# Kernel tuning notes

Hardware: AMD Instinct MI355X
Metric: run time of the kernel (lower is better)

Reference implementation:

```python
import jax, jax.numpy as jnp
import numpy as np

NB = 16   # num_blocks
DIN = 64  # per-block input dim
DOUT = 64 # per-block output dim
NT = 2    # n_templates (ns)


def setup_inputs() -> dict:
    key = jax.random.key(0)
    k1, k2, k3, k4, k5 = jax.random.split(key, 5)
    T, B = 2048, 8
    a = 0.1  # GroupLinearLayer init range
    x = jax.random.normal(k1, (T, B, NB * DIN), dtype=jnp.float32)
    module_emb = 0.1 * jax.random.normal(k2, (1, 1, NB * DIN), dtype=jnp.float32)
    read_w = jax.random.uniform(k3, (1, DIN, NT), dtype=jnp.float32, minval=-a, maxval=a)
    lim = 1.0 / np.sqrt(DIN)  # nn.Linear default init range
    w_stack = jax.random.uniform(k4, (NT, DOUT, DIN), dtype=jnp.float32, minval=-lim, maxval=lim)
    b_stack = jax.random.uniform(k5, (NT, DOUT), dtype=jnp.float32, minval=-lim, maxval=lim)
    return {"x": x, "module_emb": module_emb, "read_w": read_w,
            "w_stack": w_stack, "b_stack": b_stack}


def reference(x, module_emb, read_w, w_stack, b_stack):
    T, B, D = x.shape
    # add module embedding (broadcast over T, B)
    new_x = x + module_emb
    # flatten to per-block tokens: (N, DIN) with N = T*B*NB
    xf = new_x.reshape(T * B * NB, DIN)
    # routing logits via GroupLinearLayer with 1 block: (N, NT)
    logits = xf @ read_w[0]
    att = jax.nn.softmax(logits, axis=-1)
    # apply each template Linear: (N, NT, DOUT)
    x_next = jnp.einsum('nd,tod->nto', xf, w_stack) + b_stack[None, :, :]
    # soft combine templates; mean over singleton dim is identity
    out = jnp.einsum('nt,nto->no', att, x_next)
    return out.reshape(T, B, NB * DOUT)
```

## Files before the change

### kernel.cpp

```cpp
#include <hip/hip_runtime.h>


#define NBLK   768
#define WAVES  (NBLK * 4)
#define NTILES 16384

typedef short bf16x8 __attribute__((ext_vector_type(8)));
typedef float f32x4  __attribute__((ext_vector_type(4)));

union B8 { bf16x8 v; unsigned u[4]; };

__device__ __forceinline__ unsigned pk2bf(float lo, float hi) {
    unsigned a = __float_as_uint(lo) + 0x8000u;
    unsigned b = __float_as_uint(hi) + 0x8000u;
    return __builtin_amdgcn_perm(b, a, 0x07060302u);
}

__device__ __forceinline__ void pack8(B8& d, float4 p, float4 q) {
    d.u[0] = pk2bf(p.x, p.y); d.u[1] = pk2bf(p.z, p.w);
    d.u[2] = pk2bf(q.x, q.y); d.u[3] = pk2bf(q.z, q.w);
}

__global__ __launch_bounds__(256, 3) void sgll_kernel(
    const float* __restrict__ x,
    const float* __restrict__ emb,
    const float* __restrict__ rw,
    const float* __restrict__ ws,
    const float* __restrict__ bs,
    float* __restrict__ out)
{
    __shared__ bf16x8 sW1[8][64];
    __shared__ bf16x8 sWd[8][64];

    const int tid  = threadIdx.x;
    const int lane = tid & 63;
    const int wv   = tid >> 6;
    const int col  = lane & 15;
    const int q    = lane >> 4;

    #pragma unroll
    for (int c = wv; c < 8; c += 4) {
        const int kt = c >> 2, ot = c & 3;
        const float* p0 = ws + (ot * 16 + col) * 64 + kt * 32 + q * 8;
        const float* p1 = p0 + 4096;
        float4 a0 = *(const float4*)p0, a1 = *(const float4*)(p0 + 4);
        float4 c0 = *(const float4*)p1, c1 = *(const float4*)(p1 + 4);
        B8 f1, fd;
        pack8(f1, c0, c1);
        fd.u[0] = pk2bf(a0.x - c0.x, a0.y - c0.y);
        fd.u[1] = pk2bf(a0.z - c0.z, a0.w - c0.w);
        fd.u[2] = pk2bf(a1.x - c1.x, a1.y - c1.y);
        fd.u[3] = pk2bf(a1.z - c1.z, a1.w - c1.w);
        sW1[c][lane] = f1.v;
        sWd[c][lane] = fd.v;
    }

    B8 R0, R1;
    {
        const int c01 = col & 1;
        float v[8];
        #pragma unroll
        for (int j = 0; j < 8; ++j)
            v[j] = rw[(q * 8 + j) * 2 + c01];
        pack8(R0, make_float4(v[0], v[1], v[2], v[3]), make_float4(v[4], v[5], v[6], v[7]));
        #pragma unroll
        for (int j = 0; j < 8; ++j)
            v[j] = rw[(32 + q * 8 + j) * 2 + c01];
        pack8(R1, make_float4(v[0], v[1], v[2], v[3]), make_float4(v[4], v[5], v[6], v[7]));
    }

    B8 E0, E1;
    {
        const float* ep = emb + col * 64 + q * 8;
        pack8(E0, *(const float4*)ep, *(const float4*)(ep + 4));
        pack8(E1, *(const float4*)(ep + 32), *(const float4*)(ep + 36));
    }
    f32x4 bI1[4], bId[4];
    #pragma unroll
    for (int ot = 0; ot < 4; ++ot) {
        float4 b1 = *(const float4*)(bs + 64 + ot * 16 + q * 4);
        float4 b0 = *(const float4*)(bs + ot * 16 + q * 4);
        bI1[ot][0] = b1.x; bI1[ot][1] = b1.y; bI1[ot][2] = b1.z; bI1[ot][3] = b1.w;
        bId[ot][0] = b0.x - b1.x; bId[ot][1] = b0.y - b1.y;
        bId[ot][2] = b0.z - b1.z; bId[ot][3] = b0.w - b1.w;
    }

    __syncthreads();

    const int w = blockIdx.x * 4 + wv;

    auto loadt = [&](float4 (&B)[4], int T) {
        const float* p = x + ((long)T * 16 + col) * 64 + q * 8;
        B[0] = *(const float4*)p;        B[1] = *(const float4*)(p + 4);
        B[2] = *(const float4*)(p + 32); B[3] = *(const float4*)(p + 36);
    };

    float4 bA[4], bB[4], bC[4], bD[4];
    loadt(bA, w);
    loadt(bB, w + WAVES);
    loadt(bC, w + 2 * WAVES);
    loadt(bD, w + 3 * WAVES);
    __builtin_amdgcn_sched_barrier(0);

    f32x4 I1[4], Id[4], Il;
    #pragma unroll
    for (int ot = 0; ot < 4; ++ot) {
        f32x4 a1 = bI1[ot], ad = bId[ot];
        a1 = __builtin_amdgcn_mfma_f32_16x16x32_bf16(sW1[ot][lane],     E0.v, a1, 0, 0, 0);
        a1 = __builtin_amdgcn_mfma_f32_16x16x32_bf16(sW1[4 + ot][lane], E1.v, a1, 0, 0, 0);
        ad = __builtin_amdgcn_mfma_f32_16x16x32_bf16(sWd[ot][lane],     E0.v, ad, 0, 0, 0);
        ad = __builtin_amdgcn_mfma_f32_16x16x32_bf16(sWd[4 + ot][lane], E1.v, ad, 0, 0, 0);
        I1[ot] = a1;
        Id[ot] = ad;
    }
    {
        f32x4 z = {0.f, 0.f, 0.f, 0.f};
        z = __builtin_amdgcn_mfma_f32_16x16x32_bf16(R0.v, E0.v, z, 0, 0, 0);
        z = __builtin_amdgcn_mfma_f32_16x16x32_bf16(R1.v, E1.v, z, 0, 0, 0);
        Il = z;
    }

    auto step = [&](float4 (&B)[4], int TI, bool refill, int RT) {
        B8 X0, X1;
        pack8(X0, B[0], B[1]);
        pack8(X1, B[2], B[3]);
        if (refill) loadt(B, RT);

        f32x4 lac = Il;
        lac = __builtin_amdgcn_mfma_f32_16x16x32_bf16(R0.v, X0.v, lac, 0, 0, 0);
        lac = __builtin_amdgcn_mfma_f32_16x16x32_bf16(R1.v, X1.v, lac, 0, 0, 0);
        const float att = 1.0f / (1.0f + __expf(lac[1] - lac[0]));

        const long rowoff = ((long)TI * 16 + col) * 64;
        #pragma unroll
        for (int ot = 0; ot < 4; ++ot) {
            f32x4 y = I1[ot];
            y = __builtin_amdgcn_mfma_f32_16x16x32_bf16(sW1[ot][lane],     X0.v, y, 0, 0, 0);
            y = __builtin_amdgcn_mfma_f32_16x16x32_bf16(sW1[4 + ot][lane], X1.v, y, 0, 0, 0);
            f32x4 d = Id[ot];
            d = __builtin_amdgcn_mfma_f32_16x16x32_bf16(sWd[ot][lane],     X0.v, d, 0, 0, 0);
            d = __builtin_amdgcn_mfma_f32_16x16x32_bf16(sWd[4 + ot][lane], X1.v, d, 0, 0, 0);
            float4 o;
            o.x = fmaf(att, d[0], y[0]);
            o.y = fmaf(att, d[1], y[1]);
            o.z = fmaf(att, d[2], y[2]);
            o.w = fmaf(att, d[3], y[3]);
            *(float4*)(out + rowoff + ot * 16 + q * 4) = o;
        }
    };

    const bool six = (w < NTILES - 5 * WAVES);

    step(bA, w,             true, w + 4 * WAVES);
    step(bB, w +     WAVES, six,  w + 5 * WAVES);
    step(bC, w + 2 * WAVES, false, 0);
    step(bD, w + 3 * WAVES, false, 0);
    step(bA, w + 4 * WAVES, false, 0);
    if (six)
        step(bB, w + 5 * WAVES, false, 0);
}

extern "C" void kernel_launch(void* const* d_in, const int* in_sizes, int n_in,
                              void* d_out, int out_size, void* d_ws, size_t ws_size,
                              hipStream_t stream) {
    const float* x   = (const float*)d_in[0];
    const float* emb = (const float*)d_in[1];
    const float* rw  = (const float*)d_in[2];
    const float* wsk = (const float*)d_in[3];
    const float* bs  = (const float*)d_in[4];
    float* out = (float*)d_out;
    sgll_kernel<<<NBLK, 256, 0, stream>>>(x, emb, rw, wsk, bs, out);
}
```

Measured before the change: 137.5 us.

## Stage output tiles through swizzled LDS for coalesced stores, raise occupancy

Each wave now writes its 16x64 output tile into a per-wave LDS buffer with an XOR swizzle, then reads it back so each lane stores contiguous 16-byte chunks of whole rows, giving fully coalesced global writes. The prefetch depth drops from four to two tiles in flight per wave, the grid grows to 1280 blocks and launch bounds allow 5 blocks per CU, trading per-wave latency hiding for more resident waves. The extra LDS round trip adds work and 16 KB of shared memory per block, and the shallower prefetch may expose more load latency.

```diff
diff --git a/kernel.cpp b/kernel.cpp
--- a/kernel.cpp
+++ b/kernel.cpp
@@ -1,7 +1,7 @@
 #include <hip/hip_runtime.h>
 
 
-#define NBLK   768
+#define NBLK   1280
 #define WAVES  (NBLK * 4)
 #define NTILES 16384
 
@@ -21,7 +21,7 @@
     d.u[2] = pk2bf(q.x, q.y); d.u[3] = pk2bf(q.z, q.w);
 }
 
-__global__ __launch_bounds__(256, 3) void sgll_kernel(
+__global__ __launch_bounds__(256, 5) void sgll_kernel(
     const float* __restrict__ x,
     const float* __restrict__ emb,
     const float* __restrict__ rw,
@@ -31,6 +31,7 @@
 {
     __shared__ bf16x8 sW1[8][64];
     __shared__ bf16x8 sWd[8][64];
+    __shared__ float  sOut[4][1024];
 
     const int tid  = threadIdx.x;
     const int lane = tid & 63;
@@ -88,6 +89,16 @@
     __syncthreads();
 
     const int w = blockIdx.x * 4 + wv;
+    float* const sO = &sOut[wv][0];
+
+    int wo0 = col * 64 + (((0 * 4 + q) ^ col) << 2);
+    int wo1 = col * 64 + (((1 * 4 + q) ^ col) << 2);
+    int wo2 = col * 64 + (((2 * 4 + q) ^ col) << 2);
+    int wo3 = col * 64 + (((3 * 4 + q) ^ col) << 2);
+    int ro0 = (0 * 4 + q) * 64 + ((col ^ (0 * 4 + q)) << 2);
+    int ro1 = (1 * 4 + q) * 64 + ((col ^ (1 * 4 + q)) << 2);
+    int ro2 = (2 * 4 + q) * 64 + ((col ^ (2 * 4 + q)) << 2);
+    int ro3 = (3 * 4 + q) * 64 + ((col ^ (3 * 4 + q)) << 2);
 
     auto loadt = [&](float4 (&B)[4], int T) {
         const float* p = x + ((long)T * 16 + col) * 64 + q * 8;
@@ -95,11 +106,9 @@
         B[2] = *(const float4*)(p + 32); B[3] = *(const float4*)(p + 36);
     };
 
-    float4 bA[4], bB[4], bC[4], bD[4];
+    float4 bA[4], bB[4];
     loadt(bA, w);
     loadt(bB, w + WAVES);
-    loadt(bC, w + 2 * WAVES);
-    loadt(bD, w + 3 * WAVES);
     __builtin_amdgcn_sched_barrier(0);
 
     f32x4 I1[4], Id[4], Il;
@@ -131,7 +140,6 @@
         lac = __builtin_amdgcn_mfma_f32_16x16x32_bf16(R1.v, X1.v, lac, 0, 0, 0);
         const float att = 1.0f / (1.0f + __expf(lac[1] - lac[0]));
 
-        const long rowoff = ((long)TI * 16 + col) * 64;
         #pragma unroll
         for (int ot = 0; ot < 4; ++ot) {
             f32x4 y = I1[ot];
@@ -140,24 +148,33 @@
             f32x4 d = Id[ot];
             d = __builtin_amdgcn_mfma_f32_16x16x32_bf16(sWd[ot][lane],     X0.v, d, 0, 0, 0);
             d = __builtin_amdgcn_mfma_f32_16x16x32_bf16(sWd[4 + ot][lane], X1.v, d, 0, 0, 0);
-            float4 o;
-            o.x = fmaf(att, d[0], y[0]);
-            o.y = fmaf(att, d[1], y[1]);
-            o.z = fmaf(att, d[2], y[2]);
-            o.w = fmaf(att, d[3], y[3]);
-            *(float4*)(out + rowoff + ot * 16 + q * 4) = o;
+            f32x4 o;
+            o[0] = fmaf(att, d[0], y[0]);
+            o[1] = fmaf(att, d[1], y[1]);
+            o[2] = fmaf(att, d[2], y[2]);
+            o[3] = fmaf(att, d[3], y[3]);
+            const int wo = (ot == 0) ? wo0 : (ot == 1) ? wo1 : (ot == 2) ? wo2 : wo3;
+            *(f32x4*)(sO + wo) = o;
         }
+
+        f32x4 s0 = *(const f32x4*)(sO + ro0);
+        f32x4 s1 = *(const f32x4*)(sO + ro1);
+        f32x4 s2 = *(const f32x4*)(sO + ro2);
+        f32x4 s3 = *(const f32x4*)(sO + ro3);
+        float* gp = out + (long)TI * 1024 + lane * 4;
+        *(f32x4*)(gp)       = s0;
+        *(f32x4*)(gp + 256) = s1;
+        *(f32x4*)(gp + 512) = s2;
+        *(f32x4*)(gp + 768) = s3;
     };
 
-    const bool six = (w < NTILES - 5 * WAVES);
+    const bool four = (w < NTILES - 3 * WAVES);
 
-    step(bA, w,             true, w + 4 * WAVES);
-    step(bB, w +     WAVES, six,  w + 5 * WAVES);
-    step(bC, w + 2 * WAVES, false, 0);
-    step(bD, w + 3 * WAVES, false, 0);
-    step(bA, w + 4 * WAVES, false, 0);
-    if (six)
-        step(bB, w + 5 * WAVES, false, 0);
+    step(bA, w,             true, w + 2 * WAVES);
+    step(bB, w +     WAVES, four, w + 3 * WAVES);
+    step(bA, w + 2 * WAVES, false, 0);
+    if (four)
+        step(bB, w + 3 * WAVES, false, 0);
 }
 
 extern "C" void kernel_launch(void* const* d_in, const int* in_sizes, int n_in,
```

After: 208.8 us. 51.9% more time.

## Process one tile per wave with a larger grid instead of a persistent multi-tile loop

Applied to the files above, without the earlier changes.

The launch now uses 4096 blocks, so each wave handles exactly one 16-row tile instead of the 768-block persistent layout where each wave stepped through five or six tiles with register prefetch buffers. The x load is issued first, before the weight staging and bias/embedding setup, so it overlaps that setup. Fewer live registers permit raising the launch bound to 6 blocks per SM for more occupancy. The cost is that every block repeats the weight staging, the embedding and bias MFMAs and the barrier, and cross-tile prefetch pipelining within a wave is lost.

```diff
diff --git a/kernel.cpp b/kernel.cpp
--- a/kernel.cpp
+++ b/kernel.cpp
@@ -1,9 +1,7 @@
 #include <hip/hip_runtime.h>
 
 
-#define NBLK   768
-#define WAVES  (NBLK * 4)
-#define NTILES 16384
+#define NBLK 4096
 
 typedef short bf16x8 __attribute__((ext_vector_type(8)));
 typedef float f32x4  __attribute__((ext_vector_type(4)));
@@ -21,7 +19,7 @@
     d.u[2] = pk2bf(q.x, q.y); d.u[3] = pk2bf(q.z, q.w);
 }
 
-__global__ __launch_bounds__(256, 3) void sgll_kernel(
+__global__ __launch_bounds__(256, 6) void sgll_kernel(
     const float* __restrict__ x,
     const float* __restrict__ emb,
     const float* __restrict__ rw,
@@ -37,6 +35,15 @@
     const int wv   = tid >> 6;
     const int col  = lane & 15;
     const int q    = lane >> 4;
+
+    const int w = blockIdx.x * 4 + wv;
+
+    const float* xp = x + ((long)w * 16 + col) * 64 + q * 8;
+    float4 xb0 = *(const float4*)xp;
+    float4 xb1 = *(const float4*)(xp + 4);
+    float4 xb2 = *(const float4*)(xp + 32);
+    float4 xb3 = *(const float4*)(xp + 36);
+    __builtin_amdgcn_sched_barrier(0);
 
     #pragma unroll
     for (int c = wv; c < 8; c += 4) {
@@ -87,21 +94,6 @@
 
     __syncthreads();
 
-    const int w = blockIdx.x * 4 + wv;
-
-    auto loadt = [&](float4 (&B)[4], int T) {
-        const float* p = x + ((long)T * 16 + col) * 64 + q * 8;
-        B[0] = *(const float4*)p;        B[1] = *(const float4*)(p + 4);
-        B[2] = *(const float4*)(p + 32); B[3] = *(const float4*)(p + 36);
-    };
-
-    float4 bA[4], bB[4], bC[4], bD[4];
-    loadt(bA, w);
-    loadt(bB, w + WAVES);
-    loadt(bC, w + 2 * WAVES);
-    loadt(bD, w + 3 * WAVES);
-    __builtin_amdgcn_sched_barrier(0);
-
     f32x4 I1[4], Id[4], Il;
     #pragma unroll
     for (int ot = 0; ot < 4; ++ot) {
@@ -120,44 +112,31 @@
         Il = z;
     }
 
-    auto step = [&](float4 (&B)[4], int TI, bool refill, int RT) {
-        B8 X0, X1;
-        pack8(X0, B[0], B[1]);
-        pack8(X1, B[2], B[3]);
-        if (refill) loadt(B, RT);
+    B8 X0, X1;
+    pack8(X0, xb0, xb1);
+    pack8(X1, xb2, xb3);
 
-        f32x4 lac = Il;
-        lac = __builtin_amdgcn_mfma_f32_16x16x32_bf16(R0.v, X0.v, lac, 0, 0, 0);
-        lac = __builtin_amdgcn_mfma_f32_16x16x32_bf16(R1.v, X1.v, lac, 0, 0, 0);
-        const float att = 1.0f / (1.0f + __expf(lac[1] - lac[0]));
+    f32x4 lac = Il;
+    lac = __builtin_amdgcn_mfma_f32_16x16x32_bf16(R0.v, X0.v, lac, 0, 0, 0);
+    lac = __builtin_amdgcn_mfma_f32_16x16x32_bf16(R1.v, X1.v, lac, 0, 0, 0);
+    const float att = 1.0f / (1.0f + __expf(lac[1] - lac[0]));
 
-        const long rowoff = ((long)TI * 16 + col) * 64;
-        #pragma unroll
-        for (int ot = 0; ot < 4; ++ot) {
-            f32x4 y = I1[ot];
-            y = __builtin_amdgcn_mfma_f32_16x16x32_bf16(sW1[ot][lane],     X0.v, y, 0, 0, 0);
-            y = __builtin_amdgcn_mfma_f32_16x16x32_bf16(sW1[4 + ot][lane], X1.v, y, 0, 0, 0);
-            f32x4 d = Id[ot];
-            d = __builtin_amdgcn_mfma_f32_16x16x32_bf16(sWd[ot][lane],     X0.v, d, 0, 0, 0);
-            d = __builtin_amdgcn_mfma_f32_16x16x32_bf16(sWd[4 + ot][lane], X1.v, d, 0, 0, 0);
-            float4 o;
-            o.x = fmaf(att, d[0], y[0]);
-            o.y = fmaf(att, d[1], y[1]);
-            o.z = fmaf(att, d[2], y[2]);
-            o.w = fmaf(att, d[3], y[3]);
-            *(float4*)(out + rowoff + ot * 16 + q * 4) = o;
-        }
-    };
-
-    const bool six = (w < NTILES - 5 * WAVES);
-
-    step(bA, w,             true, w + 4 * WAVES);
-    step(bB, w +     WAVES, six,  w + 5 * WAVES);
-    step(bC, w + 2 * WAVES, false, 0);
-    step(bD, w + 3 * WAVES, false, 0);
-    step(bA, w + 4 * WAVES, false, 0);
-    if (six)
-        step(bB, w + 5 * WAVES, false, 0);
+    const long rowoff = ((long)w * 16 + col) * 64;
+    #pragma unroll
+    for (int ot = 0; ot < 4; ++ot) {
+        f32x4 y = I1[ot];
+        y = __builtin_amdgcn_mfma_f32_16x16x32_bf16(sW1[ot][lane],     X0.v, y, 0, 0, 0);
+        y = __builtin_amdgcn_mfma_f32_16x16x32_bf16(sW1[4 + ot][lane], X1.v, y, 0, 0, 0);
+        f32x4 d = Id[ot];
+        d = __builtin_amdgcn_mfma_f32_16x16x32_bf16(sWd[ot][lane],     X0.v, d, 0, 0, 0);
+        d = __builtin_amdgcn_mfma_f32_16x16x32_bf16(sWd[4 + ot][lane], X1.v, d, 0, 0, 0);
+        float4 o;
+        o.x = fmaf(att, d[0], y[0]);
+        o.y = fmaf(att, d[1], y[1]);
+        o.z = fmaf(att, d[2], y[2]);
+        o.w = fmaf(att, d[3], y[3]);
+        *(float4*)(out + rowoff + ot * 16 + q * 4) = o;
+    }
 }
 
 extern "C" void kernel_launch(void* const* d_in, const int* in_sizes, int n_in,
```

Result: slower. 184.1 us (+33.9%).
